# Kernel tuning notes

Measured on AMD Instinct MI355X. Metric: run time of the kernel, lower is better.

## Reference

```python
import jax, jax.numpy as jnp
import numpy as np

N = 50000
E = 800000
IN_C = 256
HID = 256
OUT_C = 64
HEADS = 4
NEG_SLOPE = 0.2  # PyG GATConv default leaky_relu slope


def gat_conv(x, edge_index, W, a_src, a_dst, bias, heads, concat):
    """PyG-style GATConv (add_self_loops=True, eval mode so no dropout).
    x: [N, F_in]; W: [F_in, heads*C]; a_src/a_dst: [heads, C]; bias: [heads*C] or [C].
    """
    n = x.shape[0]
    # add self loops
    loops = jnp.arange(n, dtype=edge_index.dtype)
    src = jnp.concatenate([edge_index[0], loops])
    dst = jnp.concatenate([edge_index[1], loops])
    h = (x @ W).reshape(n, heads, -1)               # [N, H, C]
    alpha_src = jnp.einsum('nhc,hc->nh', h, a_src)  # [N, H]
    alpha_dst = jnp.einsum('nhc,hc->nh', h, a_dst)
    e = jax.nn.leaky_relu(alpha_src[src] + alpha_dst[dst], NEG_SLOPE)  # [E', H]
    # segment softmax over incoming edges of each dst node
    m = jax.ops.segment_max(e, dst, num_segments=n)        # [N, H]
    w = jnp.exp(e - m[dst])
    denom = jax.ops.segment_sum(w, dst, num_segments=n)    # [N, H]
    att = w / (denom[dst] + 1e-16)                          # [E', H]
    out = jax.ops.segment_sum(h[src] * att[:, :, None], dst, num_segments=n)  # [N, H, C]
    out = out.reshape(n, -1) if concat else out.mean(axis=1)
    return out + bias


def setup_inputs() -> dict:
    key = jax.random.key(0)
    ks = jax.random.split(key, 10)
    c1 = HID // HEADS  # per-head channels of layer 1
    s_in = 1.0 / np.sqrt(IN_C)
    s_hid = 1.0 / np.sqrt(HID)
    return {
        'x': jax.random.normal(ks[0], (N, IN_C), dtype=jnp.float32),
        'edge_index': jax.random.randint(ks[1], (2, E), 0, N, dtype=jnp.int64),
        'W1': jax.random.normal(ks[2], (IN_C, HEADS * c1), dtype=jnp.float32) * s_in,
        'a_src1': jax.random.normal(ks[3], (HEADS, c1), dtype=jnp.float32) * s_in,
        'a_dst1': jax.random.normal(ks[4], (HEADS, c1), dtype=jnp.float32) * s_in,
        'b1': jnp.zeros((HEADS * c1,), dtype=jnp.float32),
        'W2': jax.random.normal(ks[5], (HID, OUT_C), dtype=jnp.float32) * s_hid,
        'a_src2': jax.random.normal(ks[6], (1, OUT_C), dtype=jnp.float32) * s_hid,
        'a_dst2': jax.random.normal(ks[7], (1, OUT_C), dtype=jnp.float32) * s_hid,
        'b2': jnp.zeros((OUT_C,), dtype=jnp.float32),
    }


def reference(x, edge_index, W1, a_src1, a_dst1, b1, W2, a_src2, a_dst2, b2):
    h = gat_conv(x, edge_index, W1, a_src1, a_dst1, b1, heads=HEADS, concat=True)
    h = jax.nn.elu(h)
    # dropout: eval mode -> identity
    return gat_conv(h, edge_index, W2, a_src2, a_dst2, b2, heads=1, concat=False)
```

## Files before the change

kernel.cpp:

```cpp
#include <hip/hip_runtime.h>
#include <math.h>

#define NN 50000
#define NE 800000
#define ET (NE + NN)
#define FIN 256
#define HIDC 256
#define OC 64
#define NH 4
#define NEG 0.2f
#define CAP 64
#define NSTRIPES (NN / 16)
#define NGROUPS ((NSTRIPES + 1) / 2)

typedef __attribute__((ext_vector_type(8))) short bf16x8;
typedef __attribute__((ext_vector_type(4))) float f32x4;

__device__ __forceinline__ unsigned short f2bf(float f) {
    unsigned u = __float_as_uint(f);
    unsigned r = (u + 0x7FFFu + ((u >> 16) & 1u)) >> 16;
    return (unsigned short)r;
}
__device__ __forceinline__ float bflo(unsigned v) { return __uint_as_float(v << 16); }
__device__ __forceinline__ float bfhi(unsigned v) { return __uint_as_float(v & 0xffff0000u); }

__global__ void k_scatter(const int* __restrict__ ei, int* __restrict__ cnt,
                          unsigned short* __restrict__ esrc) {
    int e = blockIdx.x * blockDim.x + threadIdx.x;
    if (e >= ET) return;
    int s, d;
    if (e < NE) { s = ei[e]; d = ei[NE + e]; } else { s = d = e - NE; }
    int k = atomicAdd(&cnt[d], 1);
    if (k < CAP) esrc[(size_t)d * CAP + k] = (unsigned short)s;
}

__global__ void k_cvt(const float* __restrict__ x, unsigned short* __restrict__ xb,
                      int n) {
    int i = (blockIdx.x * 256 + threadIdx.x) * 8;
    if (i >= n) return;
    float4 f0 = *(const float4*)&x[i];
    float4 f1 = *(const float4*)&x[i + 4];
    uint4 o;
    o.x = (unsigned)f2bf(f0.x) | ((unsigned)f2bf(f0.y) << 16);
    o.y = (unsigned)f2bf(f0.z) | ((unsigned)f2bf(f0.w) << 16);
    o.z = (unsigned)f2bf(f1.x) | ((unsigned)f2bf(f1.y) << 16);
    o.w = (unsigned)f2bf(f1.z) | ((unsigned)f2bf(f1.w) << 16);
    *(uint4*)&xb[i] = o;
}

__global__ void k_pack(const float* __restrict__ W, unsigned short* __restrict__ Bp,
                       int N, int NTL, int total) {
    int t = blockIdx.x * 256 + threadIdx.x;
    if (t >= total) return;
    int lane = t & 63;
    int ntl = (t >> 6) % NTL;
    int ks = ((t >> 6) / NTL) & 7;
    int hy = t / (64 * NTL * 8);
    int col = hy * NTL * 16 + ntl * 16 + (lane & 15);
    int k0 = ks * 32 + (lane >> 4) * 8;
#pragma unroll
    for (int i = 0; i < 8; i++) Bp[(size_t)t * 8 + i] = f2bf(W[(k0 + i) * N + col]);
}

template <int NTL, int NHEADS>
__global__ void __launch_bounds__(256) k_gemm(const unsigned short* __restrict__ A,
                                              const unsigned short* __restrict__ Bp,
                                              unsigned short* __restrict__ D, int N,
                                              const float* __restrict__ aS,
                                              const float* __restrict__ aD,
                                              float* __restrict__ asOut,
                                              float* __restrict__ adOut) {
    constexpr int TOT = 8 * NTL * 64 * 8;
    constexpr int HPH = (NTL * 16) / 64;
    const unsigned short* bsrc = Bp + (size_t)blockIdx.y * TOT;
    int wave = threadIdx.x >> 6, lane = threadIdx.x & 63;
    int l15 = lane & 15, lh = lane >> 4;
    int coloff = blockIdx.y * NTL * 16;
    float aSv[NTL], aDv[NTL];
#pragma unroll
    for (int nt = 0; nt < NTL; nt++) {
        aSv[nt] = aS[coloff + nt * 16 + l15];
        aDv[nt] = aD[coloff + nt * 16 + l15];
    }
    for (int g = blockIdx.x * 4 + wave; g < NGROUPS; g += gridDim.x * 4) {
        int st0 = g * 2;
        bool two = (st0 + 1 < NSTRIPES);
        const unsigned short* arow0 = A + (size_t)(st0 * 16 + l15) * 256 + lh * 8;
        const unsigned short* arow1 = two ? arow0 + 16 * 256 : arow0;
        bf16x8 a0[8], a1[8];
#pragma unroll
        for (int ks = 0; ks < 8; ks++) a0[ks] = *(const bf16x8*)(arow0 + ks * 32);
#pragma unroll
        for (int ks = 0; ks < 8; ks++) a1[ks] = *(const bf16x8*)(arow1 + ks * 32);
        f32x4 acc[2][NTL];
#pragma unroll
        for (int m = 0; m < 2; m++)
#pragma unroll
            for (int t = 0; t < NTL; t++) acc[m][t] = (f32x4){0.f, 0.f, 0.f, 0.f};
#pragma unroll
        for (int ks = 0; ks < 8; ks++) {
#pragma unroll
            for (int nt = 0; nt < NTL; nt++) {
                bf16x8 b = *(const bf16x8*)&bsrc[((size_t)(ks * NTL + nt) * 64 + lane) * 8];
                acc[0][nt] = __builtin_amdgcn_mfma_f32_16x16x32_bf16(a0[ks], b, acc[0][nt], 0, 0, 0);
                acc[1][nt] = __builtin_amdgcn_mfma_f32_16x16x32_bf16(a1[ks], b, acc[1][nt], 0, 0, 0);
            }
        }
        int nm = two ? 2 : 1;
        for (int m = 0; m < nm; m++) {
            int strow = (st0 + m) * 16;
            unsigned short* dbase = D + (size_t)strow * N + coloff;
#pragma unroll
            for (int nt = 0; nt < NTL; nt++)
#pragma unroll
                for (int r = 0; r < 4; r++)
                    dbase[(lh * 4 + r) * N + nt * 16 + l15] = f2bf(acc[m][nt][r]);
#pragma unroll
            for (int r = 0; r < 4; r++) {
#pragma unroll
                for (int gg = 0; gg < HPH; gg++) {
                    float ps = 0.f, pd = 0.f;
#pragma unroll
                    for (int q = 0; q < 4; q++) {
                        int nt = gg * 4 + q;
                        ps += acc[m][nt][r] * aSv[nt];
                        pd += acc[m][nt][r] * aDv[nt];
                    }
#pragma unroll
                    for (int off = 1; off < 16; off <<= 1) {
                        ps += __shfl_xor(ps, off);
                        pd += __shfl_xor(pd, off);
                    }
                    if (l15 == 0) {
                        int row = strow + lh * 4 + r;
                        int hidx = blockIdx.y * HPH + gg;
                        asOut[row * NHEADS + hidx] = ps;
                        adOut[row * NHEADS + hidx] = pd;
                    }
                }
            }
        }
    }
}


__global__ void k_agg1f(const int* __restrict__ cnt, const unsigned short* __restrict__ esrc,
                        const unsigned short* __restrict__ h, const float* __restrict__ as,
                        const float* __restrict__ ad, const float* __restrict__ bias,
                        unsigned short* __restrict__ out) {
    __shared__ float wlds[4][64][4];
    int wave = threadIdx.x >> 6;
    int n = blockIdx.x * 4 + wave;
    int lane = threadIdx.x & 63;
    if (n >= NN) return;
    int deg = cnt[n];
    deg = deg < CAP ? deg : CAP;
    const unsigned short* bucket = &esrc[(size_t)n * CAP];
    bool act = lane < deg;
    int myS = act ? (int)bucket[lane] : 0;
    float4 adv = *(const float4*)&ad[n * NH];
    float e0 = -INFINITY, e1 = -INFINITY, e2 = -INFINITY, e3 = -INFINITY;
    if (act) {
        float4 av = *(const float4*)&as[myS * NH];
        e0 = av.x + adv.x; e0 = e0 > 0.f ? e0 : NEG * e0;
        e1 = av.y + adv.y; e1 = e1 > 0.f ? e1 : NEG * e1;
        e2 = av.z + adv.z; e2 = e2 > 0.f ? e2 : NEG * e2;
        e3 = av.w + adv.w; e3 = e3 > 0.f ? e3 : NEG * e3;
    }
    float m0 = e0, m1 = e1, m2 = e2, m3 = e3;
    for (int off = 32; off; off >>= 1) {
        m0 = fmaxf(m0, __shfl_xor(m0, off));
        m1 = fmaxf(m1, __shfl_xor(m1, off));
        m2 = fmaxf(m2, __shfl_xor(m2, off));
        m3 = fmaxf(m3, __shfl_xor(m3, off));
    }
    float w0 = act ? expf(e0 - m0) : 0.f;
    float w1 = act ? expf(e1 - m1) : 0.f;
    float w2 = act ? expf(e2 - m2) : 0.f;
    float w3 = act ? expf(e3 - m3) : 0.f;
    *(float4*)&wlds[wave][lane][0] = (float4){w0, w1, w2, w3};
    float s0 = w0, s1 = w1, s2 = w2, s3 = w3;
    for (int off = 32; off; off >>= 1) {
        s0 += __shfl_xor(s0, off);
        s1 += __shfl_xor(s1, off);
        s2 += __shfl_xor(s2, off);
        s3 += __shfl_xor(s3, off);
    }
    int hh = lane >> 4;
    int cbase = hh * 64 + (lane & 15) * 4;
    float ssel = hh == 0 ? s0 : hh == 1 ? s1 : hh == 2 ? s2 : s3;
    float rsel = 1.f / (ssel + 1e-16f);
    const float* wcol = &wlds[wave][0][hh];
    const unsigned short* hb = h + cbase;
    float acc0 = 0.f, acc1 = 0.f, acc2 = 0.f, acc3 = 0.f;
    int degP = (deg + 7) & ~7;
    for (int j = 0; j < degP; j += 8) {
        uint2 pv[8];
        float wj[8];
#pragma unroll
        for (int u = 0; u < 8; u++) {
            int s = __shfl(myS, j + u);
            wj[u] = wcol[(j + u) * 4];
            pv[u] = *(const uint2*)&hb[(size_t)s * HIDC];
        }
#pragma unroll
        for (int u = 0; u < 8; u++) {
            acc0 += wj[u] * bflo(pv[u].x);
            acc1 += wj[u] * bfhi(pv[u].x);
            acc2 += wj[u] * bflo(pv[u].y);
            acc3 += wj[u] * bfhi(pv[u].y);
        }
    }
    float4 bv = *(const float4*)&bias[cbase];
    float v0 = acc0 * rsel + bv.x; v0 = v0 > 0.f ? v0 : expm1f(v0);
    float v1 = acc1 * rsel + bv.y; v1 = v1 > 0.f ? v1 : expm1f(v1);
    float v2 = acc2 * rsel + bv.z; v2 = v2 > 0.f ? v2 : expm1f(v2);
    float v3 = acc3 * rsel + bv.w; v3 = v3 > 0.f ? v3 : expm1f(v3);
    uint2 ov;
    ov.x = (unsigned)f2bf(v0) | ((unsigned)f2bf(v1) << 16);
    ov.y = (unsigned)f2bf(v2) | ((unsigned)f2bf(v3) << 16);
    *(uint2*)&out[(size_t)n * HIDC + cbase] = ov;
}

__global__ void k_agg2f(const int* __restrict__ cnt, const unsigned short* __restrict__ esrc,
                        const unsigned short* __restrict__ h, const float* __restrict__ as,
                        const float* __restrict__ ad, const float* __restrict__ bias,
                        float* __restrict__ out) {
    __shared__ float wlds[4][64];
    int wave = threadIdx.x >> 6;
    int n = blockIdx.x * 4 + wave;
    int lane = threadIdx.x & 63;
    if (n >= NN) return;
    int deg = cnt[n];
    deg = deg < CAP ? deg : CAP;
    const unsigned short* bucket = &esrc[(size_t)n * CAP];
    bool act = lane < deg;
    int myS = act ? (int)bucket[lane] : 0;
    float adv = ad[n];
    float e = -INFINITY;
    if (act) {
        e = as[myS] + adv;
        e = e > 0.f ? e : NEG * e;
    }
    float m = e;
    for (int off = 32; off; off >>= 1) m = fmaxf(m, __shfl_xor(m, off));
    float w = act ? expf(e - m) : 0.f;
    wlds[wave][lane] = w;
    float s = w;
    for (int off = 32; off; off >>= 1) s += __shfl_xor(s, off);
    float rd = 1.f / (s + 1e-16f);

    int sub = lane >> 4;
    int cw = (lane & 15) * 4;
    const unsigned short* hb = h + cw;
    float acc0 = 0.f, acc1 = 0.f, acc2 = 0.f, acc3 = 0.f;
    int degP = (deg + 7) & ~7;
    for (int j = 0; j < degP; j += 8) {
        uint2 pv[2];
        float wj[2];
#pragma unroll
        for (int u = 0; u < 2; u++) {
            int jj = j + u * 4 + sub;
            int sj = __shfl(myS, jj);
            wj[u] = wlds[wave][jj];
            pv[u] = *(const uint2*)&hb[(size_t)sj * OC];
        }
#pragma unroll
        for (int u = 0; u < 2; u++) {
            acc0 += wj[u] * bflo(pv[u].x);
            acc1 += wj[u] * bfhi(pv[u].x);
            acc2 += wj[u] * bflo(pv[u].y);
            acc3 += wj[u] * bfhi(pv[u].y);
        }
    }
#pragma unroll
    for (int off = 16; off < 64; off <<= 1) {
        acc0 += __shfl_xor(acc0, off);
        acc1 += __shfl_xor(acc1, off);
        acc2 += __shfl_xor(acc2, off);
        acc3 += __shfl_xor(acc3, off);
    }
    if (lane < 16) {
        float4 bv = *(const float4*)&bias[cw];
        float4 o;
        o.x = acc0 * rd + bv.x;
        o.y = acc1 * rd + bv.y;
        o.z = acc2 * rd + bv.z;
        o.w = acc3 * rd + bv.w;
        *(float4*)&out[(size_t)n * OC + cw] = o;
    }
}

extern "C" void kernel_launch(void* const* d_in, const int* in_sizes, int n_in,
                              void* d_out, int out_size, void* d_ws, size_t ws_size,
                              hipStream_t stream) {
    const float* x   = (const float*)d_in[0];
    const int*   ei  = (const int*)d_in[1];
    const float* W1  = (const float*)d_in[2];
    const float* aS1 = (const float*)d_in[3];
    const float* aD1 = (const float*)d_in[4];
    const float* b1  = (const float*)d_in[5];
    const float* W2  = (const float*)d_in[6];
    const float* aS2 = (const float*)d_in[7];
    const float* aD2 = (const float*)d_in[8];
    const float* b2  = (const float*)d_in[9];
    float* out = (float*)d_out;

    char* p = (char*)d_ws;
    auto alloc = [&](size_t nbytes) {
        char* r = p;
        p += (nbytes + 255) & ~(size_t)255;
        return r;
    };
    unsigned short* xb    = (unsigned short*)alloc((size_t)NN * FIN * 2);
    unsigned short* h1b   = (unsigned short*)alloc((size_t)NN * HIDC * 2);
    unsigned short* act1b = (unsigned short*)alloc((size_t)NN * HIDC * 2);
    unsigned short* h2b   = (unsigned short*)alloc((size_t)NN * OC * 2);
    unsigned short* Bp1   = (unsigned short*)alloc((size_t)2 * 8 * 8 * 64 * 8 * 2);
    unsigned short* Bp2   = (unsigned short*)alloc((size_t)1 * 8 * 4 * 64 * 8 * 2);
    float* as1  = (float*)alloc((size_t)NN * NH * 4);
    float* ad1  = (float*)alloc((size_t)NN * NH * 4);
    float* as2  = (float*)alloc((size_t)NN * 4);
    float* ad2  = (float*)alloc((size_t)NN * 4);
    int*   cnt  = (int*)alloc((size_t)NN * 4);
    unsigned short* esrc = (unsigned short*)alloc((size_t)NN * CAP * 2);

    hipMemsetAsync(cnt, 0, (size_t)NN * 4, stream);

    k_scatter<<<(ET + 255) / 256, 256, 0, stream>>>(ei, cnt, esrc);
    k_cvt<<<(NN * FIN / 8 + 255) / 256, 256, 0, stream>>>(x, xb, NN * FIN);
    k_pack<<<(2 * 8 * 8 * 64 + 255) / 256, 256, 0, stream>>>(W1, Bp1, HIDC, 8, 2 * 8 * 8 * 64);
    k_pack<<<(1 * 8 * 4 * 64 + 255) / 256, 256, 0, stream>>>(W2, Bp2, OC, 4, 1 * 8 * 4 * 64);

    k_gemm<8, NH><<<dim3(256, 2), 256, 0, stream>>>(xb, Bp1, h1b, HIDC, aS1, aD1, as1, ad1);
    k_agg1f<<<(NN + 3) / 4, 256, 0, stream>>>(cnt, esrc, h1b, as1, ad1, b1, act1b);

    k_gemm<4, 1><<<dim3(256, 1), 256, 0, stream>>>(act1b, Bp2, h2b, OC, aS2, aD2, as2, ad2);
    k_agg2f<<<(NN + 3) / 4, 256, 0, stream>>>(cnt, esrc, h2b, as2, ad2, b2, out);
}
```

Measured before the change: 218.7 us.

## Fuse prep kernels, restructure layer-1 aggregation per column slice, regrid GEMMs

Merges the scatter, bf16 conversion and two weight-pack kernels into one block-dispatched prep launch to save launch overhead. Rewrites the layer-1 aggregation as a persistent kernel where each block owns one 32-column slice of a head. Each wave handles one node, with 8 lane groups splitting edges and combining partial sums by shuffle. The GEMM grids change from 256 to 391 blocks in x. The aggregation change trades extra shuffles and repeated softmax work per slice for narrower, more cache-friendly gathers.

```diff
diff --git a/kernel.cpp b/kernel.cpp
--- a/kernel.cpp
+++ b/kernel.cpp
@@ -24,34 +24,14 @@
 __device__ __forceinline__ float bflo(unsigned v) { return __uint_as_float(v << 16); }
 __device__ __forceinline__ float bfhi(unsigned v) { return __uint_as_float(v & 0xffff0000u); }
 
-__global__ void k_scatter(const int* __restrict__ ei, int* __restrict__ cnt,
-                          unsigned short* __restrict__ esrc) {
-    int e = blockIdx.x * blockDim.x + threadIdx.x;
-    if (e >= ET) return;
-    int s, d;
-    if (e < NE) { s = ei[e]; d = ei[NE + e]; } else { s = d = e - NE; }
-    int k = atomicAdd(&cnt[d], 1);
-    if (k < CAP) esrc[(size_t)d * CAP + k] = (unsigned short)s;
-}
-
-__global__ void k_cvt(const float* __restrict__ x, unsigned short* __restrict__ xb,
-                      int n) {
-    int i = (blockIdx.x * 256 + threadIdx.x) * 8;
-    if (i >= n) return;
-    float4 f0 = *(const float4*)&x[i];
-    float4 f1 = *(const float4*)&x[i + 4];
-    uint4 o;
-    o.x = (unsigned)f2bf(f0.x) | ((unsigned)f2bf(f0.y) << 16);
-    o.y = (unsigned)f2bf(f0.z) | ((unsigned)f2bf(f0.w) << 16);
-    o.z = (unsigned)f2bf(f1.x) | ((unsigned)f2bf(f1.y) << 16);
-    o.w = (unsigned)f2bf(f1.z) | ((unsigned)f2bf(f1.w) << 16);
-    *(uint4*)&xb[i] = o;
-}
-
-__global__ void k_pack(const float* __restrict__ W, unsigned short* __restrict__ Bp,
-                       int N, int NTL, int total) {
-    int t = blockIdx.x * 256 + threadIdx.x;
-    if (t >= total) return;
+#define NB_SC ((ET + 255) / 256)
+#define NB_CV (NN * FIN / 8 / 256)
+#define NB_P1 32
+#define NB_P2 8
+
+__device__ __forceinline__ void pack_body(const float* __restrict__ W,
+                                          unsigned short* __restrict__ Bp,
+                                          int N, int NTL, int t) {
     int lane = t & 63;
     int ntl = (t >> 6) % NTL;
     int ks = ((t >> 6) / NTL) & 7;
@@ -60,6 +40,36 @@
     int k0 = ks * 32 + (lane >> 4) * 8;
 #pragma unroll
     for (int i = 0; i < 8; i++) Bp[(size_t)t * 8 + i] = f2bf(W[(k0 + i) * N + col]);
+}
+
+__global__ void k_prep(const int* __restrict__ ei, int* __restrict__ cnt,
+                       unsigned short* __restrict__ esrc,
+                       const float* __restrict__ x, unsigned short* __restrict__ xb,
+                       const float* __restrict__ W1, unsigned short* __restrict__ Bp1,
+                       const float* __restrict__ W2, unsigned short* __restrict__ Bp2) {
+    int b = blockIdx.x, tid = threadIdx.x;
+    if (b < NB_SC) {
+        int e = b * 256 + tid;
+        if (e >= ET) return;
+        int s, d;
+        if (e < NE) { s = ei[e]; d = ei[NE + e]; } else { s = d = e - NE; }
+        int k = atomicAdd(&cnt[d], 1);
+        if (k < CAP) esrc[(size_t)d * CAP + k] = (unsigned short)s;
+    } else if (b < NB_SC + NB_CV) {
+        int i = ((b - NB_SC) * 256 + tid) * 8;
+        float4 f0 = *(const float4*)&x[i];
+        float4 f1 = *(const float4*)&x[i + 4];
+        uint4 o;
+        o.x = (unsigned)f2bf(f0.x) | ((unsigned)f2bf(f0.y) << 16);
+        o.y = (unsigned)f2bf(f0.z) | ((unsigned)f2bf(f0.w) << 16);
+        o.z = (unsigned)f2bf(f1.x) | ((unsigned)f2bf(f1.y) << 16);
+        o.w = (unsigned)f2bf(f1.z) | ((unsigned)f2bf(f1.w) << 16);
+        *(uint4*)&xb[i] = o;
+    } else if (b < NB_SC + NB_CV + NB_P1) {
+        pack_body(W1, Bp1, HIDC, 8, (b - NB_SC - NB_CV) * 256 + tid);
+    } else {
+        pack_body(W2, Bp2, OC, 4, (b - NB_SC - NB_CV - NB_P1) * 256 + tid);
+    }
 }
 
 template <int NTL, int NHEADS>
@@ -143,83 +153,77 @@
     }
 }
 
-
-__global__ void k_agg1f(const int* __restrict__ cnt, const unsigned short* __restrict__ esrc,
+__global__ void __launch_bounds__(256) k_agg1x(const int* __restrict__ cnt,
+                        const unsigned short* __restrict__ esrc,
                         const unsigned short* __restrict__ h, const float* __restrict__ as,
                         const float* __restrict__ ad, const float* __restrict__ bias,
                         unsigned short* __restrict__ out) {
-    __shared__ float wlds[4][64][4];
-    int wave = threadIdx.x >> 6;
-    int n = blockIdx.x * 4 + wave;
-    int lane = threadIdx.x & 63;
-    if (n >= NN) return;
-    int deg = cnt[n];
-    deg = deg < CAP ? deg : CAP;
-    const unsigned short* bucket = &esrc[(size_t)n * CAP];
-    bool act = lane < deg;
-    int myS = act ? (int)bucket[lane] : 0;
-    float4 adv = *(const float4*)&ad[n * NH];
-    float e0 = -INFINITY, e1 = -INFINITY, e2 = -INFINITY, e3 = -INFINITY;
-    if (act) {
-        float4 av = *(const float4*)&as[myS * NH];
-        e0 = av.x + adv.x; e0 = e0 > 0.f ? e0 : NEG * e0;
-        e1 = av.y + adv.y; e1 = e1 > 0.f ? e1 : NEG * e1;
-        e2 = av.z + adv.z; e2 = e2 > 0.f ? e2 : NEG * e2;
-        e3 = av.w + adv.w; e3 = e3 > 0.f ? e3 : NEG * e3;
-    }
-    float m0 = e0, m1 = e1, m2 = e2, m3 = e3;
-    for (int off = 32; off; off >>= 1) {
-        m0 = fmaxf(m0, __shfl_xor(m0, off));
-        m1 = fmaxf(m1, __shfl_xor(m1, off));
-        m2 = fmaxf(m2, __shfl_xor(m2, off));
-        m3 = fmaxf(m3, __shfl_xor(m3, off));
-    }
-    float w0 = act ? expf(e0 - m0) : 0.f;
-    float w1 = act ? expf(e1 - m1) : 0.f;
-    float w2 = act ? expf(e2 - m2) : 0.f;
-    float w3 = act ? expf(e3 - m3) : 0.f;
-    *(float4*)&wlds[wave][lane][0] = (float4){w0, w1, w2, w3};
-    float s0 = w0, s1 = w1, s2 = w2, s3 = w3;
-    for (int off = 32; off; off >>= 1) {
-        s0 += __shfl_xor(s0, off);
-        s1 += __shfl_xor(s1, off);
-        s2 += __shfl_xor(s2, off);
-        s3 += __shfl_xor(s3, off);
-    }
-    int hh = lane >> 4;
-    int cbase = hh * 64 + (lane & 15) * 4;
-    float ssel = hh == 0 ? s0 : hh == 1 ? s1 : hh == 2 ? s2 : s3;
-    float rsel = 1.f / (ssel + 1e-16f);
-    const float* wcol = &wlds[wave][0][hh];
+    __shared__ float wlds[4][64];
+    int b = blockIdx.x;
+    int slice = b & 7;
+    int hh = slice >> 1;
+    int bgrp = b >> 3;
+    int wave = threadIdx.x >> 6, lane = threadIdx.x & 63;
+    int grp = lane >> 3;
+    int cbase = slice * 32 + (lane & 7) * 4;
+    float4 bv = *(const float4*)&bias[cbase];
     const unsigned short* hb = h + cbase;
-    float acc0 = 0.f, acc1 = 0.f, acc2 = 0.f, acc3 = 0.f;
-    int degP = (deg + 7) & ~7;
-    for (int j = 0; j < degP; j += 8) {
-        uint2 pv[8];
-        float wj[8];
-#pragma unroll
-        for (int u = 0; u < 8; u++) {
-            int s = __shfl(myS, j + u);
-            wj[u] = wcol[(j + u) * 4];
-            pv[u] = *(const uint2*)&hb[(size_t)s * HIDC];
-        }
-#pragma unroll
-        for (int u = 0; u < 8; u++) {
-            acc0 += wj[u] * bflo(pv[u].x);
-            acc1 += wj[u] * bfhi(pv[u].x);
-            acc2 += wj[u] * bflo(pv[u].y);
-            acc3 += wj[u] * bfhi(pv[u].y);
-        }
-    }
-    float4 bv = *(const float4*)&bias[cbase];
-    float v0 = acc0 * rsel + bv.x; v0 = v0 > 0.f ? v0 : expm1f(v0);
-    float v1 = acc1 * rsel + bv.y; v1 = v1 > 0.f ? v1 : expm1f(v1);
-    float v2 = acc2 * rsel + bv.z; v2 = v2 > 0.f ? v2 : expm1f(v2);
-    float v3 = acc3 * rsel + bv.w; v3 = v3 > 0.f ? v3 : expm1f(v3);
-    uint2 ov;
-    ov.x = (unsigned)f2bf(v0) | ((unsigned)f2bf(v1) << 16);
-    ov.y = (unsigned)f2bf(v2) | ((unsigned)f2bf(v3) << 16);
-    *(uint2*)&out[(size_t)n * HIDC + cbase] = ov;
+    for (int n = bgrp * 4 + wave; n < NN; n += 512) {
+        int deg = cnt[n];
+        deg = deg < CAP ? deg : CAP;
+        const unsigned short* bucket = &esrc[(size_t)n * CAP];
+        bool act = lane < deg;
+        int myS = act ? (int)bucket[lane] : 0;
+        float e = -INFINITY;
+        if (act) {
+            e = as[myS * NH + hh] + ad[n * NH + hh];
+            e = e > 0.f ? e : NEG * e;
+        }
+        float m = e;
+        for (int off = 32; off; off >>= 1) m = fmaxf(m, __shfl_xor(m, off));
+        float w = act ? expf(e - m) : 0.f;
+        wlds[wave][lane] = w;
+        float ssum = w;
+        for (int off = 32; off; off >>= 1) ssum += __shfl_xor(ssum, off);
+        float rsel = 1.f / (ssum + 1e-16f);
+        float a0 = 0.f, a1 = 0.f, a2 = 0.f, a3 = 0.f;
+        int degP = (deg + 15) & ~15;
+        for (int j = 0; j < degP; j += 16) {
+            uint2 pv[2];
+            float wj[2];
+#pragma unroll
+            for (int u = 0; u < 2; u++) {
+                int jj = j + u * 8 + grp;
+                int sj = __shfl(myS, jj);
+                wj[u] = wlds[wave][jj];
+                pv[u] = *(const uint2*)&hb[(size_t)sj * HIDC];
+            }
+#pragma unroll
+            for (int u = 0; u < 2; u++) {
+                a0 += wj[u] * bflo(pv[u].x);
+                a1 += wj[u] * bfhi(pv[u].x);
+                a2 += wj[u] * bflo(pv[u].y);
+                a3 += wj[u] * bfhi(pv[u].y);
+            }
+        }
+#pragma unroll
+        for (int off = 8; off < 64; off <<= 1) {
+            a0 += __shfl_xor(a0, off);
+            a1 += __shfl_xor(a1, off);
+            a2 += __shfl_xor(a2, off);
+            a3 += __shfl_xor(a3, off);
+        }
+        if (grp == 0) {
+            float v0 = a0 * rsel + bv.x; v0 = v0 > 0.f ? v0 : expm1f(v0);
+            float v1 = a1 * rsel + bv.y; v1 = v1 > 0.f ? v1 : expm1f(v1);
+            float v2 = a2 * rsel + bv.z; v2 = v2 > 0.f ? v2 : expm1f(v2);
+            float v3 = a3 * rsel + bv.w; v3 = v3 > 0.f ? v3 : expm1f(v3);
+            uint2 ov;
+            ov.x = (unsigned)f2bf(v0) | ((unsigned)f2bf(v1) << 16);
+            ov.y = (unsigned)f2bf(v2) | ((unsigned)f2bf(v3) << 16);
+            *(uint2*)&out[(size_t)n * HIDC + cbase] = ov;
+        }
+    }
 }
 
 __global__ void k_agg2f(const int* __restrict__ cnt, const unsigned short* __restrict__ esrc,
@@ -327,14 +331,12 @@
 
     hipMemsetAsync(cnt, 0, (size_t)NN * 4, stream);
 
-    k_scatter<<<(ET + 255) / 256, 256, 0, stream>>>(ei, cnt, esrc);
-    k_cvt<<<(NN * FIN / 8 + 255) / 256, 256, 0, stream>>>(x, xb, NN * FIN);
-    k_pack<<<(2 * 8 * 8 * 64 + 255) / 256, 256, 0, stream>>>(W1, Bp1, HIDC, 8, 2 * 8 * 8 * 64);
-    k_pack<<<(1 * 8 * 4 * 64 + 255) / 256, 256, 0, stream>>>(W2, Bp2, OC, 4, 1 * 8 * 4 * 64);
-
-    k_gemm<8, NH><<<dim3(256, 2), 256, 0, stream>>>(xb, Bp1, h1b, HIDC, aS1, aD1, as1, ad1);
-    k_agg1f<<<(NN + 3) / 4, 256, 0, stream>>>(cnt, esrc, h1b, as1, ad1, b1, act1b);
-
-    k_gemm<4, 1><<<dim3(256, 1), 256, 0, stream>>>(act1b, Bp2, h2b, OC, aS2, aD2, as2, ad2);
+    k_prep<<<NB_SC + NB_CV + NB_P1 + NB_P2, 256, 0, stream>>>(ei, cnt, esrc, x, xb,
+                                                              W1, Bp1, W2, Bp2);
+
+    k_gemm<8, NH><<<dim3(391, 2), 256, 0, stream>>>(xb, Bp1, h1b, HIDC, aS1, aD1, as1, ad1);
+    k_agg1x<<<1024, 256, 0, stream>>>(cnt, esrc, h1b, as1, ad1, b1, act1b);
+
+    k_gemm<4, 1><<<dim3(391, 1), 256, 0, stream>>>(act1b, Bp2, h2b, OC, aS2, aD2, as2, ad2);
     k_agg2f<<<(NN + 3) / 4, 256, 0, stream>>>(cnt, esrc, h2b, as2, ad2, b2, out);
 }
```

New measurement: 407.3 us. 86.2% more time.
